# Performance work log

Hardware: AMD Instinct MI355X
Metric: run time of the kernel (lower is better)

## Reference

```python
import jax, jax.numpy as jnp
import numpy as np

EPS_NORM = 1e-6
EPS_LN = 1e-5


def setup_inputs() -> dict:
    key = jax.random.key(0)
    ks = jax.random.split(key, 6)
    b, m, d = 8, 1024, 768
    n, p = 64, 16
    h = 2 * d
    x = jax.random.normal(ks[0], (b, m, d), dtype=jnp.float32)
    phi = jax.random.normal(ks[1], (n, p, d), dtype=jnp.float32)
    # per-expert LayerNorm affine params
    ln_g = jnp.ones((n, d), dtype=jnp.float32)
    ln_b = jnp.zeros((n, d), dtype=jnp.float32)
    # per-expert MLP weights (torch Linear default init ~ U(-1/sqrt(fan_in), ...); use scaled normal)
    w1 = jax.random.normal(ks[2], (n, d, h), dtype=jnp.float32) * (1.0 / np.sqrt(d))
    b1 = jax.random.normal(ks[3], (n, h), dtype=jnp.float32) * 0.01
    w2 = jax.random.normal(ks[4], (n, h, d), dtype=jnp.float32) * (1.0 / np.sqrt(h))
    b2 = jax.random.normal(ks[5], (n, d), dtype=jnp.float32) * 0.01
    return {"x": x, "phi": phi, "ln_g": ln_g, "ln_b": ln_b,
            "w1": w1, "b1": b1, "w2": w2, "b2": b2}


def _layernorm(x, g, b):
    mu = jnp.mean(x, axis=-1, keepdims=True)
    var = jnp.mean(jnp.square(x - mu), axis=-1, keepdims=True)
    return (x - mu) * jax.lax.rsqrt(var + EPS_LN) * g + b


def reference(x, phi, ln_g, ln_b, w1, b1, w2, b2):
    # normalize phi over axis=0 (expert axis), as in the torch __init__
    phi_n = phi * jax.lax.rsqrt(jnp.sum(jnp.square(phi), axis=0, keepdims=True) + EPS_NORM)
    bsz, m, d = x.shape
    n, p, _ = phi_n.shape
    # routing logits: [b, m, n, p]
    logits = jnp.einsum('bmd,npd->bmnp', x, phi_n)
    # dispatch: softmax over tokens m
    D = jax.nn.softmax(logits, axis=1)
    # combine: softmax over flattened slots (n*p)
    C = jax.nn.softmax(logits.reshape(bsz, m, n * p), axis=-1)
    # input slots: [b, n, p, d]
    Xs = jnp.einsum('bmd,bmnp->bnpd', x, D)
    # batched per-expert MLP: LN -> Linear -> GELU -> Linear
    hdn = _layernorm(Xs, ln_g[:, None, :], ln_b[:, None, :])
    hdn = jnp.einsum('bnpd,ndh->bnph', hdn, w1) + b1[:, None, :]
    hdn = jax.nn.gelu(hdn, approximate=False)
    Ys = jnp.einsum('bnph,nhd->bnpd', hdn, w2) + b2[:, None, :]
    # combine: [b, m, d]
    Ys = Ys.reshape(bsz, n * p, d)
    Y = jnp.einsum('bsd,bms->bmd', Ys, C)
    return Y
```

## Files before the change

### kernel.cpp

```cpp
#include <hip/hip_runtime.h>
#include <math.h>

#define B 8
#define M 1024
#define D 768
#define NEXP 64
#define P 16
#define H 1536
#define S 1024
#define EPS_NORM 1e-6f
#define EPS_LN   1e-5f

typedef unsigned short u16;
typedef __attribute__((ext_vector_type(8))) short bf16x8;
typedef __attribute__((ext_vector_type(4))) float f32x4;

__device__ __forceinline__ u16 f2bf(float f) {
    union { float f; unsigned u; } v; v.f = f;
    unsigned r = v.u + 0x7FFFu + ((v.u >> 16) & 1u);
    return (u16)(r >> 16);
}

__device__ __forceinline__ float gelu_exact(float x) {
    return 0.5f * x * (1.0f + erff(x * 0.70710678118654752440f));
}

#define GLL16(g, l) __builtin_amdgcn_global_load_lds( \
    (const __attribute__((address_space(1))) void*)(g), \
    (__attribute__((address_space(3))) void*)(l), 16, 0, 0)

__device__ __forceinline__ void mfma_core_128(const u16* __restrict__ Ag,
                                              const u16* __restrict__ Bg,
                                              int K, u16* As, u16* Bs,
                                              f32x4 (&acc)[4][4]) {
    const int t    = threadIdx.x;
    const int lane = t & 63;
    const int wave = t >> 6;
    const int wr   = (wave >> 1) << 6;
    const int wc   = (wave & 1) << 6;
    const int quad = lane >> 4;
    const int l16  = lane & 15;
    const u16* ga0 = Ag + (size_t)(t >> 2) * K + (t & 3) * 8;
    const u16* ga1 = ga0 + (size_t)64 * K;
    const u16* gb0 = Bg + (size_t)(t >> 2) * K + (t & 3) * 8;
    const u16* gb1 = gb0 + (size_t)64 * K;
    u16* la0 = As + t * 8;
    u16* lb0 = Bs + t * 8;
    const u16* arp = As + (wr + l16) * 32 + quad * 8;
    const u16* brp = Bs + (wc + l16) * 32 + quad * 8;
    GLL16(ga0, la0);
    GLL16(ga1, la0 + 2048);
    GLL16(gb0, lb0);
    GLL16(gb1, lb0 + 2048);
    int cur = 0;
    for (int k0 = 0; k0 < K; k0 += 32) {
        __syncthreads();
        const int nxt = cur ^ 1;
        if (k0 + 32 < K) {
            GLL16(ga0 + k0 + 32, la0 + nxt * 4096);
            GLL16(ga1 + k0 + 32, la0 + nxt * 4096 + 2048);
            GLL16(gb0 + k0 + 32, lb0 + nxt * 4096);
            GLL16(gb1 + k0 + 32, lb0 + nxt * 4096 + 2048);
        }
        const u16* ar = arp + cur * 4096;
        const u16* br = brp + cur * 4096;
        bf16x8 af[4], bfr[4];
#pragma unroll
        for (int i = 0; i < 4; ++i) af[i]  = *(const bf16x8*)(ar + i * 512);
#pragma unroll
        for (int j = 0; j < 4; ++j) bfr[j] = *(const bf16x8*)(br + j * 512);
#pragma unroll
        for (int i = 0; i < 4; ++i)
#pragma unroll
            for (int j = 0; j < 4; ++j)
                acc[i][j] = __builtin_amdgcn_mfma_f32_16x16x32_bf16(af[i], bfr[j], acc[i][j], 0, 0, 0);
        cur = nxt;
    }
}

__device__ __forceinline__ void mfma_core_bf32(const u16* __restrict__ Ag, int K,
                                               const float* __restrict__ Bg, int ldb,
                                               u16* As, u16* Bs,
                                               f32x4 (&acc)[4][4]) {
    const int t    = threadIdx.x;
    const int lane = t & 63;
    const int wave = t >> 6;
    const int wr   = (wave >> 1) << 6;
    const int wc   = (wave & 1) << 6;
    const int quad = lane >> 4;
    const int l16  = lane & 15;
    const u16* ga0 = Ag + (size_t)(t >> 2) * K + (t & 3) * 8;
    const u16* ga1 = ga0 + (size_t)64 * K;
    u16* la0 = As + t * 8;
    const int bcol = t & 127;
    const int kq   = (t >> 7) << 4;
    const float* bg0 = Bg + (size_t)kq * ldb + bcol;
    u16* lb = Bs + bcol * 40 + kq;
    const u16* arp = As + (wr + l16) * 32 + quad * 8;
    const u16* brp = Bs + (wc + l16) * 40 + quad * 8;
    GLL16(ga0, la0);
    GLL16(ga1, la0 + 2048);
    {
        float f[16];
#pragma unroll
        for (int i = 0; i < 16; ++i) f[i] = bg0[(size_t)i * ldb];
#pragma unroll
        for (int i = 0; i < 4; ++i) {
            ushort4 o;
            o.x = f2bf(f[i*4 + 0]); o.y = f2bf(f[i*4 + 1]);
            o.z = f2bf(f[i*4 + 2]); o.w = f2bf(f[i*4 + 3]);
            *(ushort4*)(lb + i * 4) = o;
        }
    }
    int cur = 0;
    for (int k0 = 0; k0 < K; k0 += 32) {
        __syncthreads();
        const int nxt = cur ^ 1;
        const bool pf = (k0 + 32 < K);
        float f[16];
        if (pf) {
            GLL16(ga0 + k0 + 32, la0 + nxt * 4096);
            GLL16(ga1 + k0 + 32, la0 + nxt * 4096 + 2048);
            const float* bg = bg0 + (size_t)(k0 + 32) * ldb;
#pragma unroll
            for (int i = 0; i < 16; ++i) f[i] = bg[(size_t)i * ldb];
        }
        const u16* ar = arp + cur * 4096;
        const u16* br = brp + cur * 5120;
        bf16x8 af[4], bfr[4];
#pragma unroll
        for (int i = 0; i < 4; ++i) af[i]  = *(const bf16x8*)(ar + i * 512);
#pragma unroll
        for (int j = 0; j < 4; ++j) bfr[j] = *(const bf16x8*)(br + j * 640);
#pragma unroll
        for (int i = 0; i < 4; ++i)
#pragma unroll
            for (int j = 0; j < 4; ++j)
                acc[i][j] = __builtin_amdgcn_mfma_f32_16x16x32_bf16(af[i], bfr[j], acc[i][j], 0, 0, 0);
        if (pf) {
            u16* lbn = lb + nxt * 5120;
#pragma unroll
            for (int i = 0; i < 4; ++i) {
                ushort4 o;
                o.x = f2bf(f[i*4 + 0]); o.y = f2bf(f[i*4 + 1]);
                o.z = f2bf(f[i*4 + 2]); o.w = f2bf(f[i*4 + 3]);
                *(ushort4*)(lbn + i * 4) = o;
            }
        }
        cur = nxt;
    }
}

#define EPI_VARS \
    const int t = threadIdx.x; const int lane = t & 63; const int wave = t >> 6; \
    const int wr = (wave >> 1) << 6; const int wc = (wave & 1) << 6; \
    const int quad = lane >> 4; const int l16 = lane & 15; (void)t;

#define ACC_INIT \
    f32x4 acc[4][4]; \
    _Pragma("unroll") for (int i = 0; i < 4; ++i) \
    _Pragma("unroll") for (int j = 0; j < 4; ++j) acc[i][j] = (f32x4){0.f, 0.f, 0.f, 0.f};

__global__ __launch_bounds__(256) void xprep_kernel(const float* __restrict__ x,
                                                    u16* __restrict__ xb,
                                                    u16* __restrict__ xT) {
    __shared__ float tile[64][65];
    int b = blockIdx.z;
    int m0 = blockIdx.y * 64, d0 = blockIdx.x * 64;
    int tt = threadIdx.x;
    int rr = tt >> 4, c4 = (tt & 15) * 4;
#pragma unroll
    for (int i = 0; i < 4; ++i) {
        int m = m0 + rr + i * 16;
        float4 v = *(const float4*)(x + ((size_t)b * M + m) * D + d0 + c4);
        tile[rr + i*16][c4 + 0] = v.x;
        tile[rr + i*16][c4 + 1] = v.y;
        tile[rr + i*16][c4 + 2] = v.z;
        tile[rr + i*16][c4 + 3] = v.w;
        ushort4 o;
        o.x = f2bf(v.x); o.y = f2bf(v.y); o.z = f2bf(v.z); o.w = f2bf(v.w);
        *(ushort4*)(xb + ((size_t)b * M + m) * D + d0 + c4) = o;
    }
    __syncthreads();
    int cr = tt >> 4, r4 = (tt & 15) * 4;
#pragma unroll
    for (int i = 0; i < 4; ++i) {
        int crow = cr + i * 16;
        ushort4 o;
        o.x = f2bf(tile[r4 + 0][crow]);
        o.y = f2bf(tile[r4 + 1][crow]);
        o.z = f2bf(tile[r4 + 2][crow]);
        o.w = f2bf(tile[r4 + 3][crow]);
        *(ushort4*)(xT + ((size_t)b * D + d0 + crow) * M + m0 + r4) = o;
    }
}

__global__ __launch_bounds__(256) void phi_norm_kernel(const float* __restrict__ phi,
                                                       u16* __restrict__ phinb) {
    int pos = blockIdx.x * 256 + threadIdx.x;
    float ss = 0.f;
#pragma unroll 4
    for (int nn = 0; nn < NEXP; ++nn) {
        float v = phi[nn * (P*D) + pos];
        ss += v * v;
    }
    float r = rsqrtf(ss + EPS_NORM);
#pragma unroll 4
    for (int nn = 0; nn < NEXP; ++nn)
        phinb[nn * (P*D) + pos] = f2bf(phi[nn * (P*D) + pos] * r);
}


__global__ __launch_bounds__(256) void gemm_logits_mfma(const u16* __restrict__ xb,
                                                        const u16* __restrict__ phinb,
                                                        float* __restrict__ logits) {
    __shared__ __align__(16) u16 As[8192], Bs[8192];
    ACC_INIT;
    const int row0 = blockIdx.y * 128, col0 = blockIdx.x * 128;
    mfma_core_128(xb + (size_t)row0 * D, phinb + (size_t)col0 * D, D, As, Bs, acc);
    EPI_VARS;
#pragma unroll
    for (int i = 0; i < 4; ++i)
#pragma unroll
        for (int j = 0; j < 4; ++j) {
            int col = col0 + wc + j*16 + l16;
#pragma unroll
            for (int r = 0; r < 4; ++r) {
                int row = row0 + wr + i*16 + quad*4 + r;
                logits[(size_t)row * S + col] = acc[i][j][r];
            }
        }
}

__global__ __launch_bounds__(256) void gemm_dispatch_mfma(const u16* __restrict__ DT,
                                                          const u16* __restrict__ xT,
                                                          float* __restrict__ Xs) {
    __shared__ __align__(16) u16 As[8192], Bs[8192];
    ACC_INIT;
    const int b = blockIdx.z;
    const int row0 = blockIdx.y * 128, col0 = blockIdx.x * 128;
    mfma_core_128(DT + ((size_t)b * S + row0) * M,
                  xT + ((size_t)b * D + col0) * M, M, As, Bs, acc);
    EPI_VARS;
#pragma unroll
    for (int i = 0; i < 4; ++i)
#pragma unroll
        for (int j = 0; j < 4; ++j) {
            int col = col0 + wc + j*16 + l16;
#pragma unroll
            for (int r = 0; r < 4; ++r) {
                int row = row0 + wr + i*16 + quad*4 + r;
                Xs[((size_t)b * S + row) * D + col] = acc[i][j][r];
            }
        }
}

__global__ __launch_bounds__(256) void gemm_mlp1_mfma(const u16* __restrict__ hdnE,
                                                      const float* __restrict__ w1,
                                                      const float* __restrict__ b1,
                                                      u16* __restrict__ h1) {
    __shared__ __align__(16) u16 As[8192], Bs[10240];
    ACC_INIT;
    const int n = blockIdx.z;
    const int col0 = blockIdx.x * 128;
    mfma_core_bf32(hdnE + (size_t)n * 128 * D, D,
                   w1 + (size_t)n * D * H + col0, H, As, Bs, acc);
    EPI_VARS;
#pragma unroll
    for (int i = 0; i < 4; ++i)
#pragma unroll
        for (int j = 0; j < 4; ++j) {
            int h = col0 + wc + j*16 + l16;
            float bias = b1[n * H + h];
#pragma unroll
            for (int r = 0; r < 4; ++r) {
                int row = wr + i*16 + quad*4 + r;
                h1[((size_t)n * 128 + row) * H + h] = f2bf(gelu_exact(acc[i][j][r] + bias));
            }
        }
}

__global__ __launch_bounds__(256) void gemm_mlp2_mfma(const u16* __restrict__ h1,
                                                      const float* __restrict__ w2,
                                                      const float* __restrict__ b2,
                                                      u16* __restrict__ YsT) {
    __shared__ __align__(16) u16 As[8192], Bs[10240];
    ACC_INIT;
    const int n = blockIdx.z;
    const int col0 = blockIdx.x * 128;
    mfma_core_bf32(h1 + (size_t)n * 128 * H, H,
                   w2 + (size_t)n * H * D + col0, D, As, Bs, acc);
    EPI_VARS;
#pragma unroll
    for (int i = 0; i < 4; ++i)
#pragma unroll
        for (int j = 0; j < 4; ++j) {
            int d = col0 + wc + j*16 + l16;
            float bias = b2[n * D + d];
            int bb = ((wr + i*16) >> 4);
            int p0 = quad * 4;
            ushort4 o;
            o.x = f2bf(acc[i][j][0] + bias);
            o.y = f2bf(acc[i][j][1] + bias);
            o.z = f2bf(acc[i][j][2] + bias);
            o.w = f2bf(acc[i][j][3] + bias);
            *(ushort4*)(YsT + ((size_t)bb * D + d) * S + n * P + p0) = o;
        }
}

__global__ __launch_bounds__(256) void gemm_combine_mfma(const u16* __restrict__ Cb,
                                                         const u16* __restrict__ YsT,
                                                         float* __restrict__ out) {
    __shared__ __align__(16) u16 As[8192], Bs[8192];
    ACC_INIT;
    const int b = blockIdx.z;
    const int row0 = blockIdx.y * 128, col0 = blockIdx.x * 128;
    mfma_core_128(Cb + ((size_t)b * M + row0) * S,
                  YsT + ((size_t)b * D + col0) * S, S, As, Bs, acc);
    EPI_VARS;
#pragma unroll
    for (int i = 0; i < 4; ++i)
#pragma unroll
        for (int j = 0; j < 4; ++j) {
            int col = col0 + wc + j*16 + l16;
#pragma unroll
            for (int r = 0; r < 4; ++r) {
                int row = row0 + wr + i*16 + quad*4 + r;
                out[((size_t)b * M + row) * D + col] = acc[i][j][r];
            }
        }
}


__global__ __launch_bounds__(256) void softmax_row_kernel(const float* __restrict__ in,
                                                          u16* __restrict__ outb) {
    __shared__ float red[4], red2[4];
    int row = blockIdx.x;
    int t = threadIdx.x;
    const float* rp = in + (size_t)row * S;
    float4 v = *(const float4*)(rp + t*4);
    float mx = fmaxf(fmaxf(v.x, v.y), fmaxf(v.z, v.w));
#pragma unroll
    for (int o = 1; o < 64; o <<= 1) mx = fmaxf(mx, __shfl_xor(mx, o));
    if ((t & 63) == 0) red[t >> 6] = mx;
    __syncthreads();
    mx = fmaxf(fmaxf(red[0], red[1]), fmaxf(red[2], red[3]));
    float4 e;
    e.x = expf(v.x - mx); e.y = expf(v.y - mx); e.z = expf(v.z - mx); e.w = expf(v.w - mx);
    float sum = e.x + e.y + e.z + e.w;
#pragma unroll
    for (int o = 1; o < 64; o <<= 1) sum += __shfl_xor(sum, o);
    if ((t & 63) == 0) red2[t >> 6] = sum;
    __syncthreads();
    sum = red2[0] + red2[1] + red2[2] + red2[3];
    float inv = 1.f / sum;
    ushort4 o4;
    o4.x = f2bf(e.x * inv); o4.y = f2bf(e.y * inv);
    o4.z = f2bf(e.z * inv); o4.w = f2bf(e.w * inv);
    *(ushort4*)(outb + (size_t)row * S + t*4) = o4;
}

__global__ __launch_bounds__(256) void colsm_partial_kernel(const float* __restrict__ logits,
                                                            float* __restrict__ pm,
                                                            float* __restrict__ pl) {
    int gid = blockIdx.x * 256 + threadIdx.x;
    int c   = gid >> 13;
    int col = gid & 8191;
    int b = col >> 10, s = col & (S - 1);
    const float* base = logits + ((size_t)b << 20) + ((size_t)(c * 32) << 10) + s;
    float mx = -INFINITY, l = 0.f;
    for (int m = 0; m < 32; ++m) {
        float v = base[(size_t)m << 10];
        float nm = fmaxf(mx, v);
        l = l * expf(mx - nm) + expf(v - nm);
        mx = nm;
    }
    pm[gid] = mx;
    pl[gid] = l;
}

__global__ __launch_bounds__(256) void colsm_combine_kernel(const float* __restrict__ pm,
                                                            const float* __restrict__ pl,
                                                            float* __restrict__ fm,
                                                            float* __restrict__ fl) {
    int col = blockIdx.x * 256 + threadIdx.x;
    float mx = -INFINITY;
#pragma unroll
    for (int c = 0; c < 32; ++c) mx = fmaxf(mx, pm[c * 8192 + col]);
    float l = 0.f;
#pragma unroll
    for (int c = 0; c < 32; ++c) l += pl[c * 8192 + col] * expf(pm[c * 8192 + col] - mx);
    fm[col] = mx;
    fl[col] = 1.f / l;
}

__global__ __launch_bounds__(256) void dt_transpose_kernel(const float* __restrict__ logits,
                                                           const float* __restrict__ fm,
                                                           const float* __restrict__ fl,
                                                           u16* __restrict__ DT) {
    __shared__ float tile[64][65];
    int b = blockIdx.z;
    int m0 = blockIdx.y * 64, s0 = blockIdx.x * 64;
    int tt = threadIdx.x;
    int rr = tt >> 4, c4 = (tt & 15) * 4;
    float4 fmv = *(const float4*)(fm + (size_t)b * S + s0 + c4);
    float4 flv = *(const float4*)(fl + (size_t)b * S + s0 + c4);
#pragma unroll
    for (int i = 0; i < 4; ++i) {
        float4 v = *(const float4*)(logits + ((size_t)b * M + m0 + rr + i*16) * S + s0 + c4);
        tile[rr + i*16][c4 + 0] = expf(v.x - fmv.x) * flv.x;
        tile[rr + i*16][c4 + 1] = expf(v.y - fmv.y) * flv.y;
        tile[rr + i*16][c4 + 2] = expf(v.z - fmv.z) * flv.z;
        tile[rr + i*16][c4 + 3] = expf(v.w - fmv.w) * flv.w;
    }
    __syncthreads();
    int cr = tt >> 4, r4 = (tt & 15) * 4;
#pragma unroll
    for (int i = 0; i < 4; ++i) {
        int crow = cr + i * 16;
        ushort4 o;
        o.x = f2bf(tile[r4 + 0][crow]);
        o.y = f2bf(tile[r4 + 1][crow]);
        o.z = f2bf(tile[r4 + 2][crow]);
        o.w = f2bf(tile[r4 + 3][crow]);
        *(ushort4*)(DT + ((size_t)b * S + s0 + crow) * M + m0 + r4) = o;
    }
}

__global__ __launch_bounds__(256) void layernorm_kernel(const float* __restrict__ Xs,
                                                        const float* __restrict__ g,
                                                        const float* __restrict__ bt,
                                                        u16* __restrict__ hdnE) {
    __shared__ float rs[4], rq[4];
    int row = blockIdx.x;
    int b = row >> 10;
    int n = (row >> 4) & (NEXP - 1);
    int p = row & 15;
    const float* rp = Xs + (size_t)row * D;
    u16* op = hdnE + ((size_t)n * 128 + b * 16 + p) * D;
    int t = threadIdx.x;
    float x0 = rp[t], x1 = rp[t + 256], x2 = rp[t + 512];
    float s  = x0 + x1 + x2;
    float sq = x0*x0 + x1*x1 + x2*x2;
#pragma unroll
    for (int o = 1; o < 64; o <<= 1) { s += __shfl_xor(s, o); sq += __shfl_xor(sq, o); }
    if ((t & 63) == 0) { rs[t >> 6] = s; rq[t >> 6] = sq; }
    __syncthreads();
    s  = rs[0] + rs[1] + rs[2] + rs[3];
    sq = rq[0] + rq[1] + rq[2] + rq[3];
    float mu  = s * (1.f / D);
    float var = sq * (1.f / D) - mu * mu;
    float inv = rsqrtf(var + EPS_LN);
    const float* gn = g  + n * D;
    const float* bn = bt + n * D;
    op[t]       = f2bf((x0 - mu) * inv * gn[t]       + bn[t]);
    op[t + 256] = f2bf((x1 - mu) * inv * gn[t + 256] + bn[t + 256]);
    op[t + 512] = f2bf((x2 - mu) * inv * gn[t + 512] + bn[t + 512]);
}

extern "C" void kernel_launch(void* const* d_in, const int* in_sizes, int n_in,
                              void* d_out, int out_size, void* d_ws, size_t ws_size,
                              hipStream_t stream) {
    const float* x    = (const float*)d_in[0];
    const float* phi  = (const float*)d_in[1];
    const float* ln_g = (const float*)d_in[2];
    const float* ln_b = (const float*)d_in[3];
    const float* w1   = (const float*)d_in[4];
    const float* b1   = (const float*)d_in[5];
    const float* w2   = (const float*)d_in[6];
    const float* b2   = (const float*)d_in[7];
    float* out = (float*)d_out;

    char* ws = (char*)d_ws;
    float* logits = (float*)(ws + 0);
    u16*   Cb     = (u16*)(ws + 33554432);
    u16*   xb     = (u16*)(ws + 50331648);
    u16*   DT     = (u16*)(ws + 62914560);
    u16*   xTb    = (u16*)(ws + 79691776);
    u16*   phinb  = (u16*)(ws + 92274688);
    u16*   hdnE   = (u16*)(ws + 93847552);
    float* pm     = (float*)(ws + 106430464);
    float* pl     = (float*)(ws + 107479040);
    float* fm     = (float*)(ws + 108527616);
    float* fl     = (float*)(ws + 108560384);
    float* Xs     = logits;
    u16*   h1     = xb;
    u16*   YsT    = xTb;

    xprep_kernel<<<dim3(12, 16, B), 256, 0, stream>>>(x, xb, xTb);
    phi_norm_kernel<<<48, 256, 0, stream>>>(phi, phinb);

    gemm_logits_mfma<<<dim3(8, 64), 256, 0, stream>>>(xb, phinb, logits);
    softmax_row_kernel<<<B * M, 256, 0, stream>>>(logits, Cb);
    colsm_partial_kernel<<<1024, 256, 0, stream>>>(logits, pm, pl);
    colsm_combine_kernel<<<32, 256, 0, stream>>>(pm, pl, fm, fl);
    dt_transpose_kernel<<<dim3(16, 16, B), 256, 0, stream>>>(logits, fm, fl, DT);

    gemm_dispatch_mfma<<<dim3(6, 8, B), 256, 0, stream>>>(DT, xTb, Xs);
    layernorm_kernel<<<B * S, 256, 0, stream>>>(Xs, ln_g, ln_b, hdnE);

    gemm_mlp1_mfma<<<dim3(12, 1, NEXP), 256, 0, stream>>>(hdnE, w1, b1, h1);
    gemm_mlp2_mfma<<<dim3(6, 1, NEXP), 256, 0, stream>>>(h1, w2, b2, YsT);

    gemm_combine_mfma<<<dim3(6, 8, B), 256, 0, stream>>>(Cb, YsT, out);
}
```

Baseline: 800.1 us.

## Fuse prep kernels and merge row/column softmax passes over logits

Merges x preparation and phi normalization into a single launch by adding an extra grid slice. Fuses the row softmax (combine weights) with the partial column-softmax statistics, so the logits are read once for both. The column-statistic combine step moves into the dispatch-transpose kernel, where each block recomputes the final max and sum for its 64 columns. This cuts kernel launches and one full pass over the 32MB logits buffer, but the fused softmax runs only 256 blocks, each wave handling 8 rows serially, which may reduce parallelism.

```diff
diff --git a/kernel.cpp b/kernel.cpp
--- a/kernel.cpp
+++ b/kernel.cpp
@@ -161,9 +161,27 @@
     _Pragma("unroll") for (int i = 0; i < 4; ++i) \
     _Pragma("unroll") for (int j = 0; j < 4; ++j) acc[i][j] = (f32x4){0.f, 0.f, 0.f, 0.f};
 
-__global__ __launch_bounds__(256) void xprep_kernel(const float* __restrict__ x,
-                                                    u16* __restrict__ xb,
-                                                    u16* __restrict__ xT) {
+__global__ __launch_bounds__(256) void prep_fused_kernel(const float* __restrict__ x,
+                                                         const float* __restrict__ phi,
+                                                         u16* __restrict__ xb,
+                                                         u16* __restrict__ xT,
+                                                         u16* __restrict__ phinb) {
+    if (blockIdx.z == 8) {
+        int bid = blockIdx.y * 12 + blockIdx.x;
+        if (bid >= 48) return;
+        int pos = bid * 256 + threadIdx.x;
+        float ss = 0.f;
+#pragma unroll 4
+        for (int nn = 0; nn < NEXP; ++nn) {
+            float v = phi[nn * (P*D) + pos];
+            ss += v * v;
+        }
+        float r = rsqrtf(ss + EPS_NORM);
+#pragma unroll 4
+        for (int nn = 0; nn < NEXP; ++nn)
+            phinb[nn * (P*D) + pos] = f2bf(phi[nn * (P*D) + pos] * r);
+        return;
+    }
     __shared__ float tile[64][65];
     int b = blockIdx.z;
     int m0 = blockIdx.y * 64, d0 = blockIdx.x * 64;
@@ -193,21 +211,6 @@
         o.w = f2bf(tile[r4 + 3][crow]);
         *(ushort4*)(xT + ((size_t)b * D + d0 + crow) * M + m0 + r4) = o;
     }
-}
-
-__global__ __launch_bounds__(256) void phi_norm_kernel(const float* __restrict__ phi,
-                                                       u16* __restrict__ phinb) {
-    int pos = blockIdx.x * 256 + threadIdx.x;
-    float ss = 0.f;
-#pragma unroll 4
-    for (int nn = 0; nn < NEXP; ++nn) {
-        float v = phi[nn * (P*D) + pos];
-        ss += v * v;
-    }
-    float r = rsqrtf(ss + EPS_NORM);
-#pragma unroll 4
-    for (int nn = 0; nn < NEXP; ++nn)
-        phinb[nn * (P*D) + pos] = f2bf(phi[nn * (P*D) + pos] * r);
 }
 
 
@@ -331,99 +334,143 @@
         }
 }
 
-
-__global__ __launch_bounds__(256) void softmax_row_kernel(const float* __restrict__ in,
-                                                          u16* __restrict__ outb) {
-    __shared__ float red[4], red2[4];
-    int row = blockIdx.x;
-    int t = threadIdx.x;
-    const float* rp = in + (size_t)row * S;
-    float4 v = *(const float4*)(rp + t*4);
-    float mx = fmaxf(fmaxf(v.x, v.y), fmaxf(v.z, v.w));
-#pragma unroll
-    for (int o = 1; o < 64; o <<= 1) mx = fmaxf(mx, __shfl_xor(mx, o));
-    if ((t & 63) == 0) red[t >> 6] = mx;
+__global__ __launch_bounds__(256) void smcol_kernel(const float* __restrict__ logits,
+                                                    u16* __restrict__ Cb,
+                                                    float* __restrict__ pm,
+                                                    float* __restrict__ pl) {
+    __shared__ float lm[3][1024], ll[3][1024];
+    const int c2   = blockIdx.x;
+    const int b    = c2 >> 5;
+    const int mgrp = c2 & 31;
+    const int t    = threadIdx.x;
+    const int w    = t >> 6;
+    const int lane = t & 63;
+    float cm[16], cl[16];
+#pragma unroll
+    for (int i = 0; i < 16; ++i) { cm[i] = -INFINITY; cl[i] = 0.f; }
+    const size_t rbase = (size_t)(b * 1024 + mgrp * 32 + w * 8) * 1024;
+    const float* Lb = logits + rbase;
+    u16* Cbb = Cb + rbase;
+    for (int r = 0; r < 8; ++r) {
+        const float* row = Lb + (size_t)r * 1024;
+        float4 v[4];
+#pragma unroll
+        for (int q = 0; q < 4; ++q)
+            v[q] = *(const float4*)(row + q * 256 + lane * 4);
+        float mx = -INFINITY;
+#pragma unroll
+        for (int q = 0; q < 4; ++q)
+            mx = fmaxf(mx, fmaxf(fmaxf(v[q].x, v[q].y), fmaxf(v[q].z, v[q].w)));
+#pragma unroll
+        for (int o = 1; o < 64; o <<= 1) mx = fmaxf(mx, __shfl_xor(mx, o));
+        float4 e[4]; float sum = 0.f;
+#pragma unroll
+        for (int q = 0; q < 4; ++q) {
+            e[q].x = expf(v[q].x - mx); e[q].y = expf(v[q].y - mx);
+            e[q].z = expf(v[q].z - mx); e[q].w = expf(v[q].w - mx);
+            sum += e[q].x + e[q].y + e[q].z + e[q].w;
+        }
+#pragma unroll
+        for (int o = 1; o < 64; o <<= 1) sum += __shfl_xor(sum, o);
+        float inv = 1.f / sum;
+#pragma unroll
+        for (int q = 0; q < 4; ++q) {
+            ushort4 o4;
+            o4.x = f2bf(e[q].x * inv); o4.y = f2bf(e[q].y * inv);
+            o4.z = f2bf(e[q].z * inv); o4.w = f2bf(e[q].w * inv);
+            *(ushort4*)(Cbb + (size_t)r * 1024 + q * 256 + lane * 4) = o4;
+        }
+#pragma unroll
+        for (int q = 0; q < 4; ++q) {
+            float vv[4] = {v[q].x, v[q].y, v[q].z, v[q].w};
+#pragma unroll
+            for (int j = 0; j < 4; ++j) {
+                int idx = q * 4 + j;
+                float nm = fmaxf(cm[idx], vv[j]);
+                cl[idx] = cl[idx] * expf(cm[idx] - nm) + expf(vv[j] - nm);
+                cm[idx] = nm;
+            }
+        }
+    }
+    if (w > 0) {
+#pragma unroll
+        for (int q = 0; q < 4; ++q)
+#pragma unroll
+            for (int j = 0; j < 4; ++j) {
+                int col = q * 256 + lane * 4 + j;
+                lm[w - 1][col] = cm[q * 4 + j];
+                ll[w - 1][col] = cl[q * 4 + j];
+            }
+    }
     __syncthreads();
-    mx = fmaxf(fmaxf(red[0], red[1]), fmaxf(red[2], red[3]));
-    float4 e;
-    e.x = expf(v.x - mx); e.y = expf(v.y - mx); e.z = expf(v.z - mx); e.w = expf(v.w - mx);
-    float sum = e.x + e.y + e.z + e.w;
-#pragma unroll
-    for (int o = 1; o < 64; o <<= 1) sum += __shfl_xor(sum, o);
-    if ((t & 63) == 0) red2[t >> 6] = sum;
+    if (w == 0) {
+#pragma unroll
+        for (int q = 0; q < 4; ++q)
+#pragma unroll
+            for (int j = 0; j < 4; ++j) {
+                int idx = q * 4 + j;
+                int col = q * 256 + lane * 4 + j;
+#pragma unroll
+                for (int wv = 0; wv < 3; ++wv) {
+                    float m2 = lm[wv][col], l2 = ll[wv][col];
+                    float nm = fmaxf(cm[idx], m2);
+                    cl[idx] = cl[idx] * expf(cm[idx] - nm) + l2 * expf(m2 - nm);
+                    cm[idx] = nm;
+                }
+                pm[mgrp * 8192 + b * 1024 + col] = cm[idx];
+                pl[mgrp * 8192 + b * 1024 + col] = cl[idx];
+            }
+    }
+}
+
+__global__ __launch_bounds__(256) void dtc_kernel(const float* __restrict__ logits,
+                                                  const float* __restrict__ pm,
+                                                  const float* __restrict__ pl,
+                                                  u16* __restrict__ DT) {
+    __shared__ float tile[64][65];
+    __shared__ float fmS[64], flS[64];
+    const int b  = blockIdx.z;
+    const int s0 = blockIdx.x * 64;
+    const int m0base = blockIdx.y * 256;
+    const int tt = threadIdx.x;
+    if (tt < 64) {
+        int col = b * 1024 + s0 + tt;
+        float mx = -INFINITY;
+#pragma unroll 8
+        for (int c = 0; c < 32; ++c) mx = fmaxf(mx, pm[c * 8192 + col]);
+        float l = 0.f;
+#pragma unroll 8
+        for (int c = 0; c < 32; ++c) l += pl[c * 8192 + col] * expf(pm[c * 8192 + col] - mx);
+        fmS[tt] = mx;
+        flS[tt] = 1.f / l;
+    }
     __syncthreads();
-    sum = red2[0] + red2[1] + red2[2] + red2[3];
-    float inv = 1.f / sum;
-    ushort4 o4;
-    o4.x = f2bf(e.x * inv); o4.y = f2bf(e.y * inv);
-    o4.z = f2bf(e.z * inv); o4.w = f2bf(e.w * inv);
-    *(ushort4*)(outb + (size_t)row * S + t*4) = o4;
-}
-
-__global__ __launch_bounds__(256) void colsm_partial_kernel(const float* __restrict__ logits,
-                                                            float* __restrict__ pm,
-                                                            float* __restrict__ pl) {
-    int gid = blockIdx.x * 256 + threadIdx.x;
-    int c   = gid >> 13;
-    int col = gid & 8191;
-    int b = col >> 10, s = col & (S - 1);
-    const float* base = logits + ((size_t)b << 20) + ((size_t)(c * 32) << 10) + s;
-    float mx = -INFINITY, l = 0.f;
-    for (int m = 0; m < 32; ++m) {
-        float v = base[(size_t)m << 10];
-        float nm = fmaxf(mx, v);
-        l = l * expf(mx - nm) + expf(v - nm);
-        mx = nm;
-    }
-    pm[gid] = mx;
-    pl[gid] = l;
-}
-
-__global__ __launch_bounds__(256) void colsm_combine_kernel(const float* __restrict__ pm,
-                                                            const float* __restrict__ pl,
-                                                            float* __restrict__ fm,
-                                                            float* __restrict__ fl) {
-    int col = blockIdx.x * 256 + threadIdx.x;
-    float mx = -INFINITY;
-#pragma unroll
-    for (int c = 0; c < 32; ++c) mx = fmaxf(mx, pm[c * 8192 + col]);
-    float l = 0.f;
-#pragma unroll
-    for (int c = 0; c < 32; ++c) l += pl[c * 8192 + col] * expf(pm[c * 8192 + col] - mx);
-    fm[col] = mx;
-    fl[col] = 1.f / l;
-}
-
-__global__ __launch_bounds__(256) void dt_transpose_kernel(const float* __restrict__ logits,
-                                                           const float* __restrict__ fm,
-                                                           const float* __restrict__ fl,
-                                                           u16* __restrict__ DT) {
-    __shared__ float tile[64][65];
-    int b = blockIdx.z;
-    int m0 = blockIdx.y * 64, s0 = blockIdx.x * 64;
-    int tt = threadIdx.x;
-    int rr = tt >> 4, c4 = (tt & 15) * 4;
-    float4 fmv = *(const float4*)(fm + (size_t)b * S + s0 + c4);
-    float4 flv = *(const float4*)(fl + (size_t)b * S + s0 + c4);
-#pragma unroll
-    for (int i = 0; i < 4; ++i) {
-        float4 v = *(const float4*)(logits + ((size_t)b * M + m0 + rr + i*16) * S + s0 + c4);
-        tile[rr + i*16][c4 + 0] = expf(v.x - fmv.x) * flv.x;
-        tile[rr + i*16][c4 + 1] = expf(v.y - fmv.y) * flv.y;
-        tile[rr + i*16][c4 + 2] = expf(v.z - fmv.z) * flv.z;
-        tile[rr + i*16][c4 + 3] = expf(v.w - fmv.w) * flv.w;
-    }
-    __syncthreads();
-    int cr = tt >> 4, r4 = (tt & 15) * 4;
-#pragma unroll
-    for (int i = 0; i < 4; ++i) {
-        int crow = cr + i * 16;
-        ushort4 o;
-        o.x = f2bf(tile[r4 + 0][crow]);
-        o.y = f2bf(tile[r4 + 1][crow]);
-        o.z = f2bf(tile[r4 + 2][crow]);
-        o.w = f2bf(tile[r4 + 3][crow]);
-        *(ushort4*)(DT + ((size_t)b * S + s0 + crow) * M + m0 + r4) = o;
+    const int rr = tt >> 4, c4 = (tt & 15) * 4;
+    const int cr = tt >> 4, r4 = (tt & 15) * 4;
+    for (int sub = 0; sub < 4; ++sub) {
+        const int m0 = m0base + sub * 64;
+        float fm0 = fmS[c4 + 0], fm1 = fmS[c4 + 1], fm2 = fmS[c4 + 2], fm3 = fmS[c4 + 3];
+        float fl0 = flS[c4 + 0], fl1 = flS[c4 + 1], fl2 = flS[c4 + 2], fl3 = flS[c4 + 3];
+#pragma unroll
+        for (int i = 0; i < 4; ++i) {
+            float4 v = *(const float4*)(logits + ((size_t)b * M + m0 + rr + i*16) * S + s0 + c4);
+            tile[rr + i*16][c4 + 0] = expf(v.x - fm0) * fl0;
+            tile[rr + i*16][c4 + 1] = expf(v.y - fm1) * fl1;
+            tile[rr + i*16][c4 + 2] = expf(v.z - fm2) * fl2;
+            tile[rr + i*16][c4 + 3] = expf(v.w - fm3) * fl3;
+        }
+        __syncthreads();
+#pragma unroll
+        for (int i = 0; i < 4; ++i) {
+            int crow = cr + i * 16;
+            ushort4 o;
+            o.x = f2bf(tile[r4 + 0][crow]);
+            o.y = f2bf(tile[r4 + 1][crow]);
+            o.z = f2bf(tile[r4 + 2][crow]);
+            o.w = f2bf(tile[r4 + 3][crow]);
+            *(ushort4*)(DT + ((size_t)b * S + s0 + crow) * M + m0 + r4) = o;
+        }
+        __syncthreads();
     }
 }
 
@@ -481,20 +528,15 @@
     u16*   hdnE   = (u16*)(ws + 93847552);
     float* pm     = (float*)(ws + 106430464);
     float* pl     = (float*)(ws + 107479040);
-    float* fm     = (float*)(ws + 108527616);
-    float* fl     = (float*)(ws + 108560384);
     float* Xs     = logits;
     u16*   h1     = xb;
     u16*   YsT    = xTb;
 
-    xprep_kernel<<<dim3(12, 16, B), 256, 0, stream>>>(x, xb, xTb);
-    phi_norm_kernel<<<48, 256, 0, stream>>>(phi, phinb);
+    prep_fused_kernel<<<dim3(12, 16, 9), 256, 0, stream>>>(x, phi, xb, xTb, phinb);
 
     gemm_logits_mfma<<<dim3(8, 64), 256, 0, stream>>>(xb, phinb, logits);
-    softmax_row_kernel<<<B * M, 256, 0, stream>>>(logits, Cb);
-    colsm_partial_kernel<<<1024, 256, 0, stream>>>(logits, pm, pl);
-    colsm_combine_kernel<<<32, 256, 0, stream>>>(pm, pl, fm, fl);
-    dt_transpose_kernel<<<dim3(16, 16, B), 256, 0, stream>>>(logits, fm, fl, DT);
+    smcol_kernel<<<256, 256, 0, stream>>>(logits, Cb, pm, pl);
+    dtc_kernel<<<dim3(16, 4, B), 256, 0, stream>>>(logits, pm, pl, DT);
 
     gemm_dispatch_mfma<<<dim3(6, 8, B), 256, 0, stream>>>(DT, xTb, Xs);
     layernorm_kernel<<<B * S, 256, 0, stream>>>(Xs, ln_g, ln_b, hdnE);
```

Result: no change. 805.0 us (+0.6%).
